# Optimization experiments

Hardware: AMD Instinct MI355X
Metric: run time of the kernel (lower is better)

The kernel has to match this reference:

```python
import jax, jax.numpy as jnp
import numpy as np

N, E, D_IN, D, L = 50000, 800000, 128, 256, 3
BN_EPS = 1e-5


def _bn(x, gamma, beta):
    # torch BatchNorm1d training-mode forward: biased batch statistics over node dim
    m = x.mean(axis=0)
    v = x.var(axis=0)  # ddof=0, matches torch normalization
    return gamma * (x - m) * jax.lax.rsqrt(v + BN_EPS) + beta


def setup_inputs() -> dict:
    key = jax.random.key(0)
    ks = jax.random.split(key, 12)
    s_in = 1.0 / np.sqrt(D_IN)
    s_d = 1.0 / np.sqrt(D)
    s_2d = 1.0 / np.sqrt(2 * D)
    return {
        "pre_node_emb": jax.random.normal(ks[0], (1, N, D_IN), jnp.float32),
        "edge_index": jax.random.randint(ks[1], (1, E, 2), 0, N, jnp.int64),
        "W0": jax.random.uniform(ks[2], (D_IN, D), jnp.float32, -s_in, s_in),
        "b0": jax.random.uniform(ks[3], (D,), jnp.float32, -s_in, s_in),
        "W1": jax.random.uniform(ks[4], (L, D, 2 * D), jnp.float32, -s_d, s_d),
        "b1": jax.random.uniform(ks[5], (L, 2 * D), jnp.float32, -s_d, s_d),
        "g1": jnp.ones((L, 2 * D), jnp.float32),
        "beta1": jnp.zeros((L, 2 * D), jnp.float32),
        "W2": jax.random.uniform(ks[6], (L, 2 * D, D), jnp.float32, -s_2d, s_2d),
        "b2": jax.random.uniform(ks[7], (L, D), jnp.float32, -s_2d, s_2d),
        "gf": jnp.ones((L, D), jnp.float32),
        "betaf": jnp.zeros((L, D), jnp.float32),
    }


def reference(pre_node_emb, edge_index, W0, b0, W1, b1, g1, beta1, W2, b2, gf, betaf):
    x = pre_node_emb[0]            # [N, D_IN]
    ei = edge_index[0]             # [E, 2] -> transposed in torch; rows are (src, dst)
    src, dst = ei[:, 0], ei[:, 1]
    x = x @ W0 + b0                # node embedder -> [N, D]
    for l in range(L):
        # GINConv (eps=0): sum-aggregate neighbor messages, then MLP
        agg = jax.ops.segment_sum(x[src], dst, num_segments=N)   # scatter-add
        h = x + agg
        h = h @ W1[l] + b1[l]
        h = _bn(h, g1[l], beta1[l])
        h = jax.nn.relu(h)
        h = h @ W2[l] + b2[l]
        x = _bn(h + x, gf[l], betaf[l])  # residual + outer BatchNorm
    return x
```

## Files before the change

### kernel.cpp

```cpp
#include <hip/hip_runtime.h>

#define MNODES 50000
#define M_PAD  50048
#define NEDGES 800000
#define DIN    128
#define DD     256
#define D2     512
#define NLAYERS 3
#define BN_EPS 1e-5f

typedef unsigned short ushort_t;
typedef __bf16 v8bf __attribute__((ext_vector_type(8)));
typedef float  v4f  __attribute__((ext_vector_type(4)));

#define GLOBAL_AS __attribute__((address_space(1)))
#define LDS_AS    __attribute__((address_space(3)))

__device__ __forceinline__ float bf2f(ushort_t u) {
    unsigned x = ((unsigned)u) << 16;
    return __uint_as_float(x);
}
__device__ __forceinline__ ushort_t f2bf(float f) {
    unsigned u = __float_as_uint(f);
    u += 0x7FFF + ((u >> 16) & 1);
    return (ushort_t)(u >> 16);
}
__device__ __forceinline__ void async16(const ushort_t* g, ushort_t* l) {
    __builtin_amdgcn_global_load_lds((const GLOBAL_AS unsigned int*)g,
                                     (LDS_AS unsigned int*)l, 16, 0, 0);
}
#define BARRIER() asm volatile("s_barrier" ::: "memory")
#define VMWAIT4() asm volatile("s_waitcnt vmcnt(4)" ::: "memory")
#define VMWAIT0() asm volatile("s_waitcnt vmcnt(0)" ::: "memory")

#define R0 (M_PAD * DIN)
#define RW (DIN * DD + 2 * NLAYERS * DD * D2)
__global__ void k_prep_all(const float* __restrict__ pre, ushort_t* __restrict__ preb,
                           const float* __restrict__ W0, const float* __restrict__ W1,
                           const float* __restrict__ W2,
                           ushort_t* __restrict__ W0T, ushort_t* __restrict__ W1T,
                           ushort_t* __restrict__ W2T,
                           float* __restrict__ caf, float* __restrict__ ccf,
                           float* __restrict__ sums1, float* __restrict__ sumsF,
                           int* __restrict__ deg) {
    int i = blockIdx.x * blockDim.x + threadIdx.x;
    if (i < R0) {
        int row = i >> 7;
        preb[i] = f2bf(row < MNODES ? pre[i] : 0.f);
        return;
    }
    int j = i - R0;
    if (j < RW) {
        if (j < DIN * DD) {
            int n = j >> 7, k = j & 127;
            W0T[j] = f2bf(W0[k * DD + n]);
        } else if (j < DIN * DD + NLAYERS * DD * D2) {
            int j2 = j - DIN * DD;
            int l = j2 >> 17, off = j2 & 131071;
            int n = off >> 8, k = off & 255;
            W1T[(size_t)l * 131072 + off] = f2bf(W1[(size_t)l * 131072 + k * D2 + n]);
        } else {
            int j2 = j - DIN * DD - NLAYERS * DD * D2;
            int l = j2 >> 17, off = j2 & 131071;
            int n = off >> 9, k = off & 511;
            W2T[(size_t)l * 131072 + off] = f2bf(W2[(size_t)l * 131072 + k * DD + n]);
        }
        return;
    }
    j -= RW;
    if (j < 256) { caf[j] = 1.f; ccf[j] = 0.f; return; }
    j -= 256;
    if (j < 1024) { sums1[j] = 0.f; return; }
    j -= 1024;
    if (j < 512) { sumsF[j] = 0.f; return; }
    j -= 512;
    if (j < MNODES) deg[j] = 0;
}

__global__ void k_hist(const int* __restrict__ ei, int* __restrict__ deg) {
    int e = blockIdx.x * blockDim.x + threadIdx.x;
    if (e < NEDGES) atomicAdd(&deg[ei[e * 2 + 1]], 1);
}
__global__ void k_scan1(const int* __restrict__ deg, int* __restrict__ rowptr,
                        int* __restrict__ bsum, int n) {
    __shared__ int tmp[256];
    int tid = threadIdx.x;
    int i = blockIdx.x * 256 + tid;
    int v = (i < n) ? deg[i] : 0;
    tmp[tid] = v;
    __syncthreads();
    #pragma unroll
    for (int off = 1; off < 256; off <<= 1) {
        int t = (tid >= off) ? tmp[tid - off] : 0;
        __syncthreads();
        tmp[tid] += t;
        __syncthreads();
    }
    if (i < n) rowptr[i + 1] = tmp[tid];
    if (tid == 255) bsum[blockIdx.x] = tmp[255];
}
__global__ __launch_bounds__(256)
void k_scan2(int* __restrict__ bsum, int nb) {
    __shared__ int tmp[256];
    int tid = threadIdx.x;
    int v = (tid < nb) ? bsum[tid] : 0;
    tmp[tid] = v;
    __syncthreads();
    #pragma unroll
    for (int off = 1; off < 256; off <<= 1) {
        int t = (tid >= off) ? tmp[tid - off] : 0;
        __syncthreads();
        tmp[tid] += t;
        __syncthreads();
    }
    if (tid < nb) bsum[tid] = tmp[tid] - v;
}
__global__ void k_scan3(const int* __restrict__ deg, const int* __restrict__ bsum,
                        int* __restrict__ rowptr, int* __restrict__ cursor, int n) {
    int i = blockIdx.x * 256 + threadIdx.x;
    if (i == 0) rowptr[0] = 0;
    if (i < n) {
        int incl = rowptr[i + 1] + bsum[i >> 8];
        rowptr[i + 1] = incl;
        cursor[i] = incl - deg[i];
    }
}
__global__ void k_fill(const int* __restrict__ ei, int* __restrict__ cursor,
                       int* __restrict__ col) {
    int e = blockIdx.x * blockDim.x + threadIdx.x;
    if (e < NEDGES) {
        int pos = atomicAdd(&cursor[ei[e * 2 + 1]], 1);
        col[pos] = ei[e * 2];
    }
}

__global__ void k_gather(const int* __restrict__ rowptr, const int* __restrict__ col,
                         const ushort_t* __restrict__ x, const float* __restrict__ ca,
                         const float* __restrict__ cc, ushort_t* __restrict__ out) {
    int node = blockIdx.x * 4 + (threadIdx.x >> 6);
    int lane = threadIdx.x & 63;
    if (node >= MNODES) return;
    const ushort4* xp = (const ushort4*)x;
    ushort4 v = xp[(size_t)node * 64 + lane];
    float a0 = bf2f(v.x), a1 = bf2f(v.y), a2 = bf2f(v.z), a3 = bf2f(v.w);
    int s = rowptr[node], e = rowptr[node + 1];
    int i = s;
    for (; i + 7 < e; i += 8) {
        ushort4 u[8];
        #pragma unroll
        for (int j = 0; j < 8; j++) u[j] = xp[(size_t)col[i + j] * 64 + lane];
        #pragma unroll
        for (int j = 0; j < 8; j++) {
            a0 += bf2f(u[j].x); a1 += bf2f(u[j].y);
            a2 += bf2f(u[j].z); a3 += bf2f(u[j].w);
        }
    }
    for (; i < e; i++) {
        ushort4 u = xp[(size_t)col[i] * 64 + lane];
        a0 += bf2f(u.x); a1 += bf2f(u.y); a2 += bf2f(u.z); a3 += bf2f(u.w);
    }
    int c = lane * 4;
    float dn = (float)(e - s) + 1.0f;
    ushort4 o;
    o.x = f2bf(ca[c + 0] * a0 + dn * cc[c + 0]);
    o.y = f2bf(ca[c + 1] * a1 + dn * cc[c + 1]);
    o.z = f2bf(ca[c + 2] * a2 + dn * cc[c + 2]);
    o.w = f2bf(ca[c + 3] * a3 + dn * cc[c + 3]);
    ((ushort4*)out)[(size_t)node * 64 + lane] = o;
}

__global__ void k_coeffs(float* __restrict__ sums, float* __restrict__ sumsq,
                         const float* __restrict__ g, const float* __restrict__ beta,
                         float* __restrict__ ca, float* __restrict__ cc, int n) {
    int c = blockIdx.x * blockDim.x + threadIdx.x;
    if (c >= n) return;
    float mean = sums[c] * (1.0f / MNODES);
    float var  = sumsq[c] * (1.0f / MNODES) - mean * mean;
    float a    = g[c] * rsqrtf(var + BN_EPS);
    ca[c] = a;
    cc[c] = beta[c] - a * mean;
    sums[c] = 0.f;
    sumsq[c] = 0.f;
}

__global__ void k_prerelu(ushort_t* __restrict__ h, const float* __restrict__ ca,
                          const float* __restrict__ cc) {
    int i = blockIdx.x * blockDim.x + threadIdx.x;
    if (i >= MNODES * (D2 / 4)) return;
    int c = (i * 4) & (D2 - 1);
    ushort4 v = ((const ushort4*)h)[i];
    ushort4 o;
    o.x = f2bf(fmaxf(ca[c + 0] * bf2f(v.x) + cc[c + 0], 0.f));
    o.y = f2bf(fmaxf(ca[c + 1] * bf2f(v.y) + cc[c + 1], 0.f));
    o.z = f2bf(fmaxf(ca[c + 2] * bf2f(v.z) + cc[c + 2], 0.f));
    o.w = f2bf(fmaxf(ca[c + 3] * bf2f(v.w) + cc[c + 3], 0.f));
    ((ushort4*)h)[i] = o;
}

__global__ void k_apply_out(const ushort_t* __restrict__ h, const float* __restrict__ ca,
                            const float* __restrict__ cc, float* __restrict__ out) {
    int i = blockIdx.x * blockDim.x + threadIdx.x;
    if (i >= MNODES * 64) return;
    int c = (i & 63) * 4;
    ushort4 v = ((const ushort4*)h)[i];
    float4 o;
    o.x = ca[c + 0] * bf2f(v.x) + cc[c + 0];
    o.y = ca[c + 1] * bf2f(v.y) + cc[c + 1];
    o.z = ca[c + 2] * bf2f(v.z) + cc[c + 2];
    o.w = ca[c + 3] * bf2f(v.w) + cc[c + 3];
    ((float4*)out)[i] = o;
}

template<int DO_STATS, int RES>
__global__ __launch_bounds__(256, 4)
void k_gemm_bf(const ushort_t* __restrict__ A, const ushort_t* __restrict__ WT,
               const float* __restrict__ bias,
               const ushort_t* resid, const float* __restrict__ r_ca,
               const float* __restrict__ r_cc,
               ushort_t* out, float* __restrict__ sums, float* __restrict__ sumsq,
               int M, int K, int N) {
    __shared__ __align__(16) ushort_t As[2][128 * 32];
    __shared__ __align__(16) ushort_t Bs[2][128 * 32];
    const int tid = threadIdx.x;
    const int w = tid >> 6, lane = tid & 63;
    const int wm = w >> 1, wn = w & 1;
    const int quad = lane >> 4, l15 = lane & 15;
    const int m0 = blockIdx.y * 128, n0 = blockIdx.x * 128;

    const ushort_t* aA[2];
    const ushort_t* aB[2];
    int aoff[2];
    #pragma unroll
    for (int j = 0; j < 2; j++) {
        int ii = j * 4 + w;
        int r = ii * 16 + (lane >> 2);
        int cg = (lane & 3) ^ ((r >> 2) & 3);
        aA[j] = A  + (size_t)(m0 + r) * K + cg * 8;
        aB[j] = WT + (size_t)(n0 + r) * K + cg * 8;
        aoff[j] = ii * 512;
    }

    v4f acc[4][4];
    #pragma unroll
    for (int i = 0; i < 4; i++)
        #pragma unroll
        for (int j = 0; j < 4; j++)
            acc[i][j] = (v4f){0.f, 0.f, 0.f, 0.f};

    const int nk = K >> 5;

    #pragma unroll
    for (int j = 0; j < 2; j++) {
        async16(aA[j], &As[0][aoff[j]]);
        async16(aB[j], &Bs[0][aoff[j]]);
    }
    #pragma unroll
    for (int j = 0; j < 2; j++) {
        async16(aA[j] + 32, &As[1][aoff[j]]);
        async16(aB[j] + 32, &Bs[1][aoff[j]]);
    }
    VMWAIT4();
    BARRIER();

    const int sl = quad ^ ((l15 >> 2) & 3);
    for (int t = 0; t < nk; t++) {
        const ushort_t* Ab = As[t & 1];
        const ushort_t* Bb = Bs[t & 1];
        v8bf af[4], bfr[4];
        #pragma unroll
        for (int tt = 0; tt < 4; tt++) {
            int m_l = wm * 64 + tt * 16 + l15;
            af[tt]  = *(const v8bf*)&Ab[m_l * 32 + sl * 8];
            int n_l = wn * 64 + tt * 16 + l15;
            bfr[tt] = *(const v8bf*)&Bb[n_l * 32 + sl * 8];
        }
        #pragma unroll
        for (int mt = 0; mt < 4; mt++)
            #pragma unroll
            for (int nt = 0; nt < 4; nt++)
                acc[mt][nt] = __builtin_amdgcn_mfma_f32_16x16x32_bf16(
                    af[mt], bfr[nt], acc[mt][nt], 0, 0, 0);
        if (t == nk - 1) break;
        BARRIER();
        if (t + 2 < nk) {
            int kl = (t + 2) * 32;
            #pragma unroll
            for (int j = 0; j < 2; j++) {
                async16(aA[j] + kl, &As[t & 1][aoff[j]]);
                async16(aB[j] + kl, &Bs[t & 1][aoff[j]]);
            }
            VMWAIT4();
        } else {
            VMWAIT0();
        }
        BARRIER();
    }

    const int mlim = M - m0;
    float s_sum[4] = {0.f, 0.f, 0.f, 0.f}, s_sq[4] = {0.f, 0.f, 0.f, 0.f};
    #pragma unroll
    for (int nt = 0; nt < 4; nt++) {
        int colg = n0 + wn * 64 + nt * 16 + l15;
        float bia = bias[colg];
        float rca = 0.f, rcc = 0.f;
        if (RES) { rca = r_ca[colg]; rcc = r_cc[colg]; }
        #pragma unroll
        for (int mt = 0; mt < 4; mt++) {
            int rbase = wm * 64 + mt * 16 + quad * 4;
            #pragma unroll
            for (int r = 0; r < 4; r++) {
                int rl = rbase + r;
                if (rl < mlim) {
                    size_t idx = (size_t)(m0 + rl) * N + colg;
                    float v = acc[mt][nt][r] + bia;
                    if (RES) v += rca * bf2f(resid[idx]) + rcc;
                    out[idx] = f2bf(v);
                    if (DO_STATS) { s_sum[nt] += v; s_sq[nt] += v * v; }
                }
            }
        }
    }
    if (DO_STATS) {
        #pragma unroll
        for (int nt = 0; nt < 4; nt++) {
            float s = s_sum[nt], q = s_sq[nt];
            s += __shfl_xor(s, 16); q += __shfl_xor(q, 16);
            s += __shfl_xor(s, 32); q += __shfl_xor(q, 32);
            if (quad == 0) {
                int colg = n0 + wn * 64 + nt * 16 + l15;
                atomicAdd(&sums[colg], s);
                atomicAdd(&sumsq[colg], q);
            }
        }
    }
}

extern "C" void kernel_launch(void* const* d_in, const int* in_sizes, int n_in,
                              void* d_out, int out_size, void* d_ws, size_t ws_size,
                              hipStream_t stream) {
    const float* pre   = (const float*)d_in[0];
    const int*   ei    = (const int*)d_in[1];
    const float* W0    = (const float*)d_in[2];
    const float* b0    = (const float*)d_in[3];
    const float* W1    = (const float*)d_in[4];
    const float* b1    = (const float*)d_in[5];
    const float* g1    = (const float*)d_in[6];
    const float* beta1 = (const float*)d_in[7];
    const float* W2    = (const float*)d_in[8];
    const float* b2    = (const float*)d_in[9];
    const float* gf    = (const float*)d_in[10];
    const float* betaf = (const float*)d_in[11];

    char* p = (char*)d_ws;
    ushort_t* preb = (ushort_t*)p; p += (size_t)M_PAD * DIN * 2;
    ushort_t* ACT1 = (ushort_t*)p; p += (size_t)M_PAD * DD * 2;
    ushort_t* ACT2 = (ushort_t*)p; p += (size_t)M_PAD * DD * 2;
    ushort_t* H1   = (ushort_t*)p; p += (size_t)M_PAD * D2 * 2;
    ushort_t* W0T  = (ushort_t*)p; p += (size_t)DIN * DD * 2;
    ushort_t* W1T  = (ushort_t*)p; p += (size_t)NLAYERS * DD * D2 * 2;
    ushort_t* W2T  = (ushort_t*)p; p += (size_t)NLAYERS * D2 * DD * 2;
    float* sums1  = (float*)p; p += D2 * 4;
    float* sumsq1 = (float*)p; p += D2 * 4;
    float* ca1    = (float*)p; p += D2 * 4;
    float* cc1    = (float*)p; p += D2 * 4;
    float* sumsF  = (float*)p; p += DD * 4;
    float* sumsqF = (float*)p; p += DD * 4;
    float* caf    = (float*)p; p += DD * 4;
    float* ccf    = (float*)p; p += DD * 4;
    int* deg    = (int*)p; p += (size_t)MNODES * 4;
    int* rowptr = (int*)p; p += (size_t)(MNODES + 1) * 4;
    int* cursor = (int*)p; p += (size_t)MNODES * 4;
    int* colx   = (int*)p; p += (size_t)NEDGES * 4;
    int* bsum   = (int*)p; p += 256 * 4;

    dim3 blk(256);
    const int mb = (MNODES + 127) / 128;
    const int nsb = (MNODES + 255) / 256;

    const int prep_total = R0 + RW + 256 + 1024 + 512 + MNODES;
    k_prep_all<<<(prep_total + 255) / 256, blk, 0, stream>>>(
        pre, preb, W0, W1, W2, W0T, W1T, W2T, caf, ccf, sums1, sumsF, deg);

    k_hist<<<(NEDGES + 255) / 256, blk, 0, stream>>>(ei, deg);
    k_scan1<<<nsb, blk, 0, stream>>>(deg, rowptr, bsum, MNODES);
    k_scan2<<<1, blk, 0, stream>>>(bsum, nsb);
    k_scan3<<<nsb, blk, 0, stream>>>(deg, bsum, rowptr, cursor, MNODES);
    k_fill<<<(NEDGES + 255) / 256, blk, 0, stream>>>(ei, cursor, colx);

    k_gemm_bf<0, 0><<<dim3(DD / 128, mb), blk, 0, stream>>>(
        preb, W0T, b0, nullptr, nullptr, nullptr,
        ACT2, nullptr, nullptr, MNODES, DIN, DD);

    for (int l = 0; l < NLAYERS; l++) {
        k_gather<<<(MNODES + 3) / 4, blk, 0, stream>>>(rowptr, colx, ACT2, caf, ccf, ACT1);

        k_gemm_bf<1, 0><<<dim3(D2 / 128, mb), blk, 0, stream>>>(
            ACT1, W1T + (size_t)l * DD * D2, b1 + (size_t)l * D2,
            nullptr, nullptr, nullptr,
            H1, sums1, sumsq1, MNODES, DD, D2);
        k_coeffs<<<2, blk, 0, stream>>>(sums1, sumsq1, g1 + (size_t)l * D2,
                                        beta1 + (size_t)l * D2, ca1, cc1, D2);

        k_prerelu<<<(MNODES * (D2 / 4) + 255) / 256, blk, 0, stream>>>(H1, ca1, cc1);

        k_gemm_bf<1, 1><<<dim3(DD / 128, mb), blk, 0, stream>>>(
            H1, W2T + (size_t)l * D2 * DD, b2 + (size_t)l * DD,
            ACT2, caf, ccf,
            ACT2, sumsF, sumsqF, MNODES, D2, DD);
        k_coeffs<<<1, blk, 0, stream>>>(sumsF, sumsqF, gf + (size_t)l * DD,
                                        betaf + (size_t)l * DD, caf, ccf, DD);
    }

    k_apply_out<<<(MNODES * 64 + 255) / 256, blk, 0, stream>>>(ACT2, caf, ccf, (float*)d_out);
}
```

Before: 803.9 us.

## Fuse BN+ReLU into GEMM A-load, triple-buffer, swizzle blocks, replicate stat accumulators

```diff
diff --git a/kernel.cpp b/kernel.cpp
--- a/kernel.cpp
+++ b/kernel.cpp
@@ -8,9 +8,11 @@
 #define D2     512
 #define NLAYERS 3
 #define BN_EPS 1e-5f
+#define NREP   16
 
 typedef unsigned short ushort_t;
 typedef __bf16 v8bf __attribute__((ext_vector_type(8)));
+typedef unsigned short v8us __attribute__((ext_vector_type(8)));
 typedef float  v4f  __attribute__((ext_vector_type(4)));
 
 #define GLOBAL_AS __attribute__((address_space(1)))
@@ -30,19 +32,21 @@
                                      (LDS_AS unsigned int*)l, 16, 0, 0);
 }
 #define BARRIER() asm volatile("s_barrier" ::: "memory")
+#define VMWAIT8() asm volatile("s_waitcnt vmcnt(8)" ::: "memory")
 #define VMWAIT4() asm volatile("s_waitcnt vmcnt(4)" ::: "memory")
 #define VMWAIT0() asm volatile("s_waitcnt vmcnt(0)" ::: "memory")
+#define LGKM0()   asm volatile("s_waitcnt lgkmcnt(0)" ::: "memory")
 
 #define R0 (M_PAD * DIN)
 #define RW (DIN * DD + 2 * NLAYERS * DD * D2)
+#define NSTATZ (NREP * D2 * 2 + NREP * DD * 2)
 __global__ void k_prep_all(const float* __restrict__ pre, ushort_t* __restrict__ preb,
                            const float* __restrict__ W0, const float* __restrict__ W1,
                            const float* __restrict__ W2,
                            ushort_t* __restrict__ W0T, ushort_t* __restrict__ W1T,
                            ushort_t* __restrict__ W2T,
                            float* __restrict__ caf, float* __restrict__ ccf,
-                           float* __restrict__ sums1, float* __restrict__ sumsF,
-                           int* __restrict__ deg) {
+                           float* __restrict__ statz, int* __restrict__ deg) {
     int i = blockIdx.x * blockDim.x + threadIdx.x;
     if (i < R0) {
         int row = i >> 7;
@@ -70,10 +74,8 @@
     j -= RW;
     if (j < 256) { caf[j] = 1.f; ccf[j] = 0.f; return; }
     j -= 256;
-    if (j < 1024) { sums1[j] = 0.f; return; }
-    j -= 1024;
-    if (j < 512) { sumsF[j] = 0.f; return; }
-    j -= 512;
+    if (j < NSTATZ) { statz[j] = 0.f; return; }
+    j -= NSTATZ;
     if (j < MNODES) deg[j] = 0;
 }
 
@@ -171,30 +173,23 @@
 
 __global__ void k_coeffs(float* __restrict__ sums, float* __restrict__ sumsq,
                          const float* __restrict__ g, const float* __restrict__ beta,
-                         float* __restrict__ ca, float* __restrict__ cc, int n) {
+                         float* __restrict__ ca, float* __restrict__ cc,
+                         float2* __restrict__ cacc, int n) {
     int c = blockIdx.x * blockDim.x + threadIdx.x;
     if (c >= n) return;
-    float mean = sums[c] * (1.0f / MNODES);
-    float var  = sumsq[c] * (1.0f / MNODES) - mean * mean;
+    float s = 0.f, q = 0.f;
+    #pragma unroll
+    for (int r = 0; r < NREP; r++) {
+        s += sums[r * n + c];  sums[r * n + c]  = 0.f;
+        q += sumsq[r * n + c]; sumsq[r * n + c] = 0.f;
+    }
+    float mean = s * (1.0f / MNODES);
+    float var  = q * (1.0f / MNODES) - mean * mean;
     float a    = g[c] * rsqrtf(var + BN_EPS);
+    float b    = beta[c] - a * mean;
     ca[c] = a;
-    cc[c] = beta[c] - a * mean;
-    sums[c] = 0.f;
-    sumsq[c] = 0.f;
-}
-
-__global__ void k_prerelu(ushort_t* __restrict__ h, const float* __restrict__ ca,
-                          const float* __restrict__ cc) {
-    int i = blockIdx.x * blockDim.x + threadIdx.x;
-    if (i >= MNODES * (D2 / 4)) return;
-    int c = (i * 4) & (D2 - 1);
-    ushort4 v = ((const ushort4*)h)[i];
-    ushort4 o;
-    o.x = f2bf(fmaxf(ca[c + 0] * bf2f(v.x) + cc[c + 0], 0.f));
-    o.y = f2bf(fmaxf(ca[c + 1] * bf2f(v.y) + cc[c + 1], 0.f));
-    o.z = f2bf(fmaxf(ca[c + 2] * bf2f(v.z) + cc[c + 2], 0.f));
-    o.w = f2bf(fmaxf(ca[c + 3] * bf2f(v.w) + cc[c + 3], 0.f));
-    ((ushort4*)h)[i] = o;
+    cc[c] = b;
+    if (cacc) cacc[c] = make_float2(a, b);
 }
 
 __global__ void k_apply_out(const ushort_t* __restrict__ h, const float* __restrict__ ca,
@@ -211,21 +206,35 @@
     ((float4*)out)[i] = o;
 }
 
-template<int DO_STATS, int RES>
-__global__ __launch_bounds__(256, 4)
+template<int DO_STATS, int RES, int FUSE_BN>
+__global__ __launch_bounds__(256, 3)
 void k_gemm_bf(const ushort_t* __restrict__ A, const ushort_t* __restrict__ WT,
                const float* __restrict__ bias,
                const ushort_t* resid, const float* __restrict__ r_ca,
-               const float* __restrict__ r_cc,
+               const float* __restrict__ r_cc, const float2* __restrict__ cacc,
                ushort_t* out, float* __restrict__ sums, float* __restrict__ sumsq,
                int M, int K, int N) {
-    __shared__ __align__(16) ushort_t As[2][128 * 32];
-    __shared__ __align__(16) ushort_t Bs[2][128 * 32];
+    __shared__ __align__(16) ushort_t As[3][128 * 32];
+    __shared__ __align__(16) ushort_t Bs[3][128 * 32];
+    __shared__ __align__(16) float2 cacc_lds[512];
     const int tid = threadIdx.x;
     const int w = tid >> 6, lane = tid & 63;
     const int wm = w >> 1, wn = w & 1;
     const int quad = lane >> 4, l15 = lane & 15;
-    const int m0 = blockIdx.y * 128, n0 = blockIdx.x * 128;
+
+    const int nxb = N >> 7;
+    const int nwg = nxb * (int)gridDim.y;
+    const int orig = (int)blockIdx.y * nxb + (int)blockIdx.x;
+    const int qq = nwg >> 3, rr = nwg & 7, xc = orig & 7, oi = orig >> 3;
+    const int swz = (xc < rr ? xc * (qq + 1) : rr * (qq + 1) + (xc - rr) * qq) + oi;
+    const int bx = swz & (nxb - 1);
+    const int by = (nxb == 4) ? (swz >> 2) : (swz >> 1);
+    const int m0 = by * 128, n0 = bx * 128;
+
+    if (FUSE_BN) {
+        for (int k2 = tid; k2 < K; k2 += 256) cacc_lds[k2] = cacc[k2];
+        LGKM0();
+    }
 
     const ushort_t* aA[2];
     const ushort_t* aB[2];
@@ -250,22 +259,21 @@
     const int nk = K >> 5;
 
     #pragma unroll
-    for (int j = 0; j < 2; j++) {
-        async16(aA[j], &As[0][aoff[j]]);
-        async16(aB[j], &Bs[0][aoff[j]]);
-    }
-    #pragma unroll
-    for (int j = 0; j < 2; j++) {
-        async16(aA[j] + 32, &As[1][aoff[j]]);
-        async16(aB[j] + 32, &Bs[1][aoff[j]]);
-    }
-    VMWAIT4();
+    for (int s = 0; s < 3; s++) {
+        #pragma unroll
+        for (int j = 0; j < 2; j++) {
+            async16(aA[j] + s * 32, &As[s][aoff[j]]);
+            async16(aB[j] + s * 32, &Bs[s][aoff[j]]);
+        }
+    }
+    VMWAIT8();
     BARRIER();
 
     const int sl = quad ^ ((l15 >> 2) & 3);
+    int cur = 0;
     for (int t = 0; t < nk; t++) {
-        const ushort_t* Ab = As[t & 1];
-        const ushort_t* Bb = Bs[t & 1];
+        const ushort_t* Ab = As[cur];
+        const ushort_t* Bb = Bs[cur];
         v8bf af[4], bfr[4];
         #pragma unroll
         for (int tt = 0; tt < 4; tt++) {
@@ -274,6 +282,23 @@
             int n_l = wn * 64 + tt * 16 + l15;
             bfr[tt] = *(const v8bf*)&Bb[n_l * 32 + sl * 8];
         }
+        if (FUSE_BN) {
+            const float* cb = (const float*)&cacc_lds[(t << 5) + (quad << 3)];
+            float cav[8], ccv[8];
+            #pragma unroll
+            for (int j = 0; j < 8; j++) { cav[j] = cb[2 * j]; ccv[j] = cb[2 * j + 1]; }
+            #pragma unroll
+            for (int tt = 0; tt < 4; tt++) {
+                v8us au = *(v8us*)&af[tt];
+                v8us ou;
+                #pragma unroll
+                for (int j = 0; j < 8; j++) {
+                    float h = bf2f(au[j]);
+                    ou[j] = f2bf(fmaxf(fmaf(cav[j], h, ccv[j]), 0.f));
+                }
+                af[tt] = *(v8bf*)&ou;
+            }
+        }
         #pragma unroll
         for (int mt = 0; mt < 4; mt++)
             #pragma unroll
@@ -282,18 +307,21 @@
                     af[mt], bfr[nt], acc[mt][nt], 0, 0, 0);
         if (t == nk - 1) break;
         BARRIER();
-        if (t + 2 < nk) {
-            int kl = (t + 2) * 32;
+        if (t + 3 < nk) {
+            int kl = (t + 3) * 32;
             #pragma unroll
             for (int j = 0; j < 2; j++) {
-                async16(aA[j] + kl, &As[t & 1][aoff[j]]);
-                async16(aB[j] + kl, &Bs[t & 1][aoff[j]]);
+                async16(aA[j] + kl, &As[cur][aoff[j]]);
+                async16(aB[j] + kl, &Bs[cur][aoff[j]]);
             }
+            VMWAIT8();
+        } else if (t + 2 < nk) {
             VMWAIT4();
         } else {
             VMWAIT0();
         }
         BARRIER();
+        cur = (cur == 2) ? 0 : cur + 1;
     }
 
     const int mlim = M - m0;
@@ -323,14 +351,27 @@
     if (DO_STATS) {
         #pragma unroll
         for (int nt = 0; nt < 4; nt++) {
-            float s = s_sum[nt], q = s_sq[nt];
-            s += __shfl_xor(s, 16); q += __shfl_xor(q, 16);
-            s += __shfl_xor(s, 32); q += __shfl_xor(q, 32);
-            if (quad == 0) {
-                int colg = n0 + wn * 64 + nt * 16 + l15;
-                atomicAdd(&sums[colg], s);
-                atomicAdd(&sumsq[colg], q);
+            s_sum[nt] += __shfl_xor(s_sum[nt], 16); s_sq[nt] += __shfl_xor(s_sq[nt], 16);
+            s_sum[nt] += __shfl_xor(s_sum[nt], 32); s_sq[nt] += __shfl_xor(s_sq[nt], 32);
+        }
+        float* red = (float*)&As[0][0];
+        BARRIER();
+        if (quad == 0) {
+            #pragma unroll
+            for (int nt = 0; nt < 4; nt++) {
+                int cb = wn * 64 + nt * 16 + l15;
+                red[wm * 256 + cb]       = s_sum[nt];
+                red[wm * 256 + 128 + cb] = s_sq[nt];
             }
+        }
+        LGKM0();
+        BARRIER();
+        if (tid < 128) {
+            float s = red[tid]       + red[256 + tid];
+            float q = red[128 + tid] + red[384 + tid];
+            int rep = by & (NREP - 1);
+            atomicAdd(&sums[rep * N + n0 + tid], s);
+            atomicAdd(&sumsq[rep * N + n0 + tid], q);
         }
     }
 }
@@ -359,14 +400,15 @@
     ushort_t* W0T  = (ushort_t*)p; p += (size_t)DIN * DD * 2;
     ushort_t* W1T  = (ushort_t*)p; p += (size_t)NLAYERS * DD * D2 * 2;
     ushort_t* W2T  = (ushort_t*)p; p += (size_t)NLAYERS * D2 * DD * 2;
-    float* sums1  = (float*)p; p += D2 * 4;
-    float* sumsq1 = (float*)p; p += D2 * 4;
+    float* sums1  = (float*)p; p += (size_t)NREP * D2 * 4;
+    float* sumsq1 = (float*)p; p += (size_t)NREP * D2 * 4;
+    float* sumsF  = (float*)p; p += (size_t)NREP * DD * 4;
+    float* sumsqF = (float*)p; p += (size_t)NREP * DD * 4;
     float* ca1    = (float*)p; p += D2 * 4;
     float* cc1    = (float*)p; p += D2 * 4;
-    float* sumsF  = (float*)p; p += DD * 4;
-    float* sumsqF = (float*)p; p += DD * 4;
     float* caf    = (float*)p; p += DD * 4;
     float* ccf    = (float*)p; p += DD * 4;
+    float2* cacc1 = (float2*)p; p += D2 * 8;
     int* deg    = (int*)p; p += (size_t)MNODES * 4;
     int* rowptr = (int*)p; p += (size_t)(MNODES + 1) * 4;
     int* cursor = (int*)p; p += (size_t)MNODES * 4;
@@ -377,9 +419,9 @@
     const int mb = (MNODES + 127) / 128;
     const int nsb = (MNODES + 255) / 256;
 
-    const int prep_total = R0 + RW + 256 + 1024 + 512 + MNODES;
+    const int prep_total = R0 + RW + 256 + NSTATZ + MNODES;
     k_prep_all<<<(prep_total + 255) / 256, blk, 0, stream>>>(
-        pre, preb, W0, W1, W2, W0T, W1T, W2T, caf, ccf, sums1, sumsF, deg);
+        pre, preb, W0, W1, W2, W0T, W1T, W2T, caf, ccf, sums1, deg);
 
     k_hist<<<(NEDGES + 255) / 256, blk, 0, stream>>>(ei, deg);
     k_scan1<<<nsb, blk, 0, stream>>>(deg, rowptr, bsum, MNODES);
@@ -387,28 +429,26 @@
     k_scan3<<<nsb, blk, 0, stream>>>(deg, bsum, rowptr, cursor, MNODES);
     k_fill<<<(NEDGES + 255) / 256, blk, 0, stream>>>(ei, cursor, colx);
 
-    k_gemm_bf<0, 0><<<dim3(DD / 128, mb), blk, 0, stream>>>(
-        preb, W0T, b0, nullptr, nullptr, nullptr,
+    k_gemm_bf<0, 0, 0><<<dim3(DD / 128, mb), blk, 0, stream>>>(
+        preb, W0T, b0, nullptr, nullptr, nullptr, nullptr,
         ACT2, nullptr, nullptr, MNODES, DIN, DD);
 
     for (int l = 0; l < NLAYERS; l++) {
         k_gather<<<(MNODES + 3) / 4, blk, 0, stream>>>(rowptr, colx, ACT2, caf, ccf, ACT1);
 
-        k_gemm_bf<1, 0><<<dim3(D2 / 128, mb), blk, 0, stream>>>(
+        k_gemm_bf<1, 0, 0><<<dim3(D2 / 128, mb), blk, 0, stream>>>(
             ACT1, W1T + (size_t)l * DD * D2, b1 + (size_t)l * D2,
-            nullptr, nullptr, nullptr,
+            nullptr, nullptr, nullptr, nullptr,
             H1, sums1, sumsq1, MNODES, DD, D2);
         k_coeffs<<<2, blk, 0, stream>>>(sums1, sumsq1, g1 + (size_t)l * D2,
-                                        beta1 + (size_t)l * D2, ca1, cc1, D2);
-
-        k_prerelu<<<(MNODES * (D2 / 4) + 255) / 256, blk, 0, stream>>>(H1, ca1, cc1);
-
-        k_gemm_bf<1, 1><<<dim3(DD / 128, mb), blk, 0, stream>>>(
+                                        beta1 + (size_t)l * D2, ca1, cc1, cacc1, D2);
+
+        k_gemm_bf<1, 1, 1><<<dim3(DD / 128, mb), blk, 0, stream>>>(
             H1, W2T + (size_t)l * D2 * DD, b2 + (size_t)l * DD,
-            ACT2, caf, ccf,
+            ACT2, caf, ccf, cacc1,
             ACT2, sumsF, sumsqF, MNODES, D2, DD);
         k_coeffs<<<1, blk, 0, stream>>>(sumsF, sumsqF, gf + (size_t)l * DD,
-                                        betaf + (size_t)l * DD, caf, ccf, DD);
+                                        betaf + (size_t)l * DD, caf, ccf, nullptr, DD);
     }
 
     k_apply_out<<<(MNODES * 64 + 255) / 256, blk, 0, stream>>>(ACT2, caf, ccf, (float*)d_out);
```

Result: faster. 784.3 us (-2.4%).
